# Performance work log

Measured on AMD Instinct MI355X. Metric: run time of the kernel, lower is better.

Reference implementation:

```python
import jax, jax.numpy as jnp
import numpy as np

K = 20
EPS = 1e-5
NEG_SLOPE = 0.2


def _graph_feature(x, k):
    # x: [B, N, C] -> edge features [B, N, k, 2C]
    xx = jnp.sum(x * x, axis=-1)                       # [B, N]
    inner = jnp.einsum('bnc,bmc->bnm', x, x)           # [B, N, N]
    neg_dist = 2.0 * inner - xx[:, :, None] - xx[:, None, :]
    idx = jax.lax.top_k(neg_dist, k)[1]                # [B, N, k] nearest neighbors
    nbr = jax.vmap(lambda f, i: f[i])(x, idx)          # [B, N, k, C]
    center = jnp.broadcast_to(x[:, :, None, :], nbr.shape)
    return jnp.concatenate([nbr - center, center], axis=-1)


def _bn(y, gamma, beta, axes):
    mu = y.mean(axes, keepdims=True)
    var = y.var(axes, keepdims=True)
    return (y - mu) * jax.lax.rsqrt(var + EPS) * gamma + beta


def _lrelu(y):
    return jnp.where(y > 0, y, NEG_SLOPE * y)


def _edge_block(feat, w, gamma, beta):
    # feat: [B, N, k, Cin], w: [Cout, Cin] (1x1 conv)
    y = jnp.einsum('bnkc,oc->bnko', feat, w)
    y = _lrelu(_bn(y, gamma, beta, (0, 1, 2)))
    return y.max(axis=2)                               # max over k -> [B, N, Cout]


def setup_inputs() -> dict:
    key = jax.random.key(0)
    ks = jax.random.split(key, 8)
    B, N = 16, 2048
    num_features = 128
    x = jax.random.normal(ks[0], (B, N, 3), dtype=jnp.float32)
    s = 0.05
    w1 = jax.random.normal(ks[1], (64, 6), dtype=jnp.float32) * s
    w2 = jax.random.normal(ks[2], (64, 128), dtype=jnp.float32) * s
    w3 = jax.random.normal(ks[3], (128, 128), dtype=jnp.float32) * s
    w4 = jax.random.normal(ks[4], (256, 256), dtype=jnp.float32) * s
    w5 = jax.random.normal(ks[5], (512, 512), dtype=jnp.float32) * s
    we = jax.random.normal(ks[6], (num_features, 512), dtype=jnp.float32) * s
    def gb(c):
        return jnp.ones((c,), jnp.float32), jnp.zeros((c,), jnp.float32)
    g1, b1 = gb(64); g2, b2 = gb(64); g3, b3 = gb(128); g4, b4 = gb(256); g5, b5 = gb(512)
    return dict(x=x, w1=w1, g1=g1, b1=b1, w2=w2, g2=g2, b2=b2, w3=w3, g3=g3, b3=b3,
                w4=w4, g4=g4, b4=b4, w5=w5, g5=g5, b5=b5, we=we)


def reference(x, w1, g1, b1, w2, g2, b2, w3, g3, b3, w4, g4, b4, w5, g5, b5, we):
    # x: [B, N, 3]
    x1 = _edge_block(_graph_feature(x, K), w1, g1, b1)    # [B, N, 64]
    x2 = _edge_block(_graph_feature(x1, K), w2, g2, b2)   # [B, N, 64]
    x3 = _edge_block(_graph_feature(x2, K), w3, g3, b3)   # [B, N, 128]
    x4 = _edge_block(_graph_feature(x3, K), w4, g4, b4)   # [B, N, 256]
    cat = jnp.concatenate([x1, x2, x3, x4], axis=-1)      # [B, N, 512]
    y = jnp.einsum('bnc,oc->bno', cat, w5)                # conv5 (1x1 conv1d)
    y = _lrelu(_bn(y, g5, b5, (0, 1)))
    y = y.max(axis=1)                                     # global max pool -> [B, 512]
    return y @ we.T                                       # embedding -> [B, num_features]
```

## Files before the change

### kernel.cpp

```cpp
#include <hip/hip_runtime.h>
#include <hip/hip_bf16.h>
#include <cstdint>

#define B_ 16
#define N_ 2048
#define KNN_K 20
#define EPS_ 1e-5f
#define SLOPE_ 0.2f

typedef __attribute__((ext_vector_type(4))) float f32x4;
typedef __attribute__((ext_vector_type(8))) short bf16x8;

static __device__ __forceinline__ float lrelu(float v){ return v > 0.f ? v : SLOPE_*v; }

static __device__ __forceinline__ unsigned encf(float f){
  unsigned b = __float_as_uint(f);
  return (b & 0x80000000u) ? ~b : (b | 0x80000000u);
}
static __device__ __forceinline__ float decf(unsigned u){
  unsigned b = (u & 0x80000000u) ? (u ^ 0x80000000u) : ~u;
  return __uint_as_float(b);
}
static __device__ __forceinline__ short bfbits(float v){
  __hip_bfloat16 h = __float2bfloat16(v);
  return *reinterpret_cast<short*>(&h);
}
static __device__ __forceinline__ float bf2f(short s){
  __hip_bfloat16 h = *reinterpret_cast<__hip_bfloat16*>(&s);
  return __bfloat162float(h);
}

template<int C, int CP>
__global__ __launch_bounds__(256) void convert_kernel(const float* __restrict__ f, int lda,
                                                      short* __restrict__ fbf, size_t plane,
                                                      float* __restrict__ xx){
  int wid  = (blockIdx.x * 256 + threadIdx.x) >> 6;
  int lane = threadIdx.x & 63;
  if (wid >= B_*N_) return;
  const float* p = f + (size_t)wid*lda;
  float s = 0.f;
  for (int c = lane; c < CP; c += 64){
    float v = (c < C) ? p[c] : 0.f;
    short h = bfbits(v);
    float r1 = v - bf2f(h);
    short m = bfbits(r1);
    short l = bfbits(r1 - bf2f(m));
    size_t o = (size_t)wid*CP + c;
    fbf[o] = h;
    fbf[plane + o] = m;
    fbf[2*plane + o] = l;
    s += v*v;
  }
  #pragma unroll
  for (int off=32; off; off>>=1) s += __shfl_down(s, off);
  if (lane==0) xx[wid] = s;
}

template<int CP>
__global__ __launch_bounds__(256) void knn_mfma(const short* __restrict__ fbf, size_t plane,
                                                const float* __restrict__ xx,
                                                int* __restrict__ idxout){
  constexpr int SP = (CP == 32) ? 72 : CP + 8;
  constexpr int CH = CP/8;
  constexpr int KC = CP/32;
  __shared__ short fmb[3*64*SP];
  __shared__ float xn_s[64], xm_s[64];
  __shared__ float dtile[64*65];

  int b   = blockIdx.x >> 5;
  int n0  = (blockIdx.x & 31) << 6;
  int tid = threadIdx.x;
  int w    = tid >> 6;
  int lane = tid & 63;
  int fr = lane & 15, hi = lane >> 4;
  int r_loc = lane >> 2, csub = lane & 3;
  int gb = lane & 60;
  int myrow = w*16 + r_loc;
  size_t browoff = (size_t)b * N_;

  bf16x8 aH[KC], aM[KC], aL[KC];
  {
    size_t arow = (browoff + n0 + w*16 + fr) * (size_t)CP;
    #pragma unroll
    for (int kc=0; kc<KC; ++kc){
      aH[kc] = *(const bf16x8*)&fbf[arow + kc*32 + hi*8];
      aM[kc] = *(const bf16x8*)&fbf[plane + arow + kc*32 + hi*8];
      aL[kc] = *(const bf16x8*)&fbf[2*plane + arow + kc*32 + hi*8];
    }
  }
  if (tid < 64) xn_s[tid] = xx[browoff + n0 + tid];

  float sv[5]; int si[5];
  #pragma unroll
  for (int j=0;j<5;++j){ sv[j] = -1e30f; si[j] = 0x7FFFFFFF; }

  for (int mt = 0; mt < N_/64; ++mt){
    __syncthreads();
    int m0 = mt << 6;
    for (int i = tid; i < 3*64*CH; i += 256){
      int p = i / (64*CH);
      int rem = i - p*64*CH;
      int r = rem / CH, cq = rem - r*CH;
      *(bf16x8*)&fmb[p*64*SP + r*SP + cq*8] =
          *(const bf16x8*)&fbf[(size_t)p*plane + (browoff + m0 + r)*(size_t)CP + cq*8];
    }
    if (tid < 64) xm_s[tid] = xx[browoff + m0 + tid];
    __syncthreads();

    f32x4 acc[4];
    #pragma unroll
    for (int ct=0; ct<4; ++ct) acc[ct] = (f32x4){0.f,0.f,0.f,0.f};
    const short* BH = fmb;
    const short* BM = fmb + 64*SP;
    const short* BL = fmb + 2*64*SP;
    #pragma unroll
    for (int kc = 0; kc < KC; ++kc){
      #pragma unroll
      for (int ct=0; ct<4; ++ct){
        int boff = (ct*16 + fr)*SP + kc*32 + hi*8;
        bf16x8 bh = *(const bf16x8*)&BH[boff];
        bf16x8 bm = *(const bf16x8*)&BM[boff];
        bf16x8 bl = *(const bf16x8*)&BL[boff];
        acc[ct] = __builtin_amdgcn_mfma_f32_16x16x32_bf16(aH[kc], bh, acc[ct], 0,0,0);
        acc[ct] = __builtin_amdgcn_mfma_f32_16x16x32_bf16(aM[kc], bh, acc[ct], 0,0,0);
        acc[ct] = __builtin_amdgcn_mfma_f32_16x16x32_bf16(aH[kc], bm, acc[ct], 0,0,0);
        acc[ct] = __builtin_amdgcn_mfma_f32_16x16x32_bf16(aM[kc], bm, acc[ct], 0,0,0);
        acc[ct] = __builtin_amdgcn_mfma_f32_16x16x32_bf16(aL[kc], bh, acc[ct], 0,0,0);
        acc[ct] = __builtin_amdgcn_mfma_f32_16x16x32_bf16(aH[kc], bl, acc[ct], 0,0,0);
      }
    }
    #pragma unroll
    for (int reg=0; reg<4; ++reg){
      int nl = w*16 + hi*4 + reg;
      float xn = xn_s[nl];
      #pragma unroll
      for (int ct=0; ct<4; ++ct)
        dtile[nl*65 + ct*16 + fr] = 2.f*acc[ct][reg] - xn - xm_s[ct*16 + fr];
    }

    int base = myrow*65 + csub*16;
    float thr = __shfl(sv[4], lane | 3);
    unsigned qm = 0u;
    #pragma unroll
    for (int jj=0; jj<16; ++jj){
      float v = dtile[base + jj];
      qm |= (v > thr) ? (1u << jj) : 0u;
    }
    unsigned long long bal = __ballot(qm != 0u);
    while (bal){
      unsigned nib = (unsigned)((bal >> gb) & 0xFull);
      int leader = nib ? (gb + (int)__builtin_ctz(nib)) : 64;
      int bbit = (int)__builtin_ctz(qm | 0x10000u);
      float mv = dtile[base + (bbit & 15)];
      int mid = m0 + (csub << 4) + bbit;
      float cv = __shfl(mv, leader);
      int   cid = __shfl(mid, leader);
      qm = (lane == leader) ? (qm & (qm - 1u)) : qm;
      int cnt = 0;
      #pragma unroll
      for (int j=0;j<5;++j) cnt += (sv[j] >= cv) ? 1 : 0;
      cnt += __shfl_xor(cnt, 1);
      cnt += __shfl_xor(cnt, 2);
      int pos = nib ? cnt : 20;
      float pv = __shfl_up(sv[4], 1);
      int   pi = __shfl_up(si[4], 1);
      #pragma unroll
      for (int j=0;j<5;++j){
        int g = csub*5 + j;
        float ns = (g < pos) ? sv[j] : ((g == pos) ? cv : pv);
        int   ni = (g < pos) ? si[j] : ((g == pos) ? cid : pi);
        pv = sv[j]; pi = si[j];
        sv[j] = ns; si[j] = ni;
      }
      bal = __ballot(qm != 0u);
    }
  }

  size_t orow = browoff + n0 + myrow;
  #pragma unroll
  for (int j=0;j<5;++j) idxout[orow*KNN_K + csub*5 + j] = si[j];
}

template<int CP>
__global__ __launch_bounds__(256) void gemm_pq(const short* __restrict__ fbf, size_t plane,
                                               const float* __restrict__ Wsrc, int wstride, int Cin,
                                               float* __restrict__ Out, int O){
  constexpr int BK = (CP < 64) ? CP : 64;
  constexpr int SP = BK + 8;
  __shared__ short Ah[128*SP];
  __shared__ short Am[128*SP];
  __shared__ short Wh[64*SP];
  __shared__ short Wm[64*SP];
  int obl = O >> 6;
  int bo = ((int)blockIdx.x % obl) << 6;
  int bm = ((int)blockIdx.x / obl) << 7;
  int tid = threadIdx.x;
  int w = tid >> 6, lane = tid & 63;
  int fr = lane & 15, hi = lane >> 4;
  f32x4 acc[2][4];
  #pragma unroll
  for (int g=0; g<2; ++g)
    #pragma unroll
    for (int ct=0; ct<4; ++ct) acc[g][ct] = (f32x4){0.f,0.f,0.f,0.f};

  for (int k0=0; k0<CP; k0+=BK){
    __syncthreads();
    for (int i=tid; i < 128*(BK/8); i += 256){
      int r = i/(BK/8), cq = i%(BK/8);
      size_t src = ((size_t)bm + r)*CP + k0 + cq*8;
      *(bf16x8*)&Ah[r*SP + cq*8] = *(const bf16x8*)&fbf[src];
      *(bf16x8*)&Am[r*SP + cq*8] = *(const bf16x8*)&fbf[plane + src];
    }
    for (int i=tid; i < 64*(BK/8); i += 256){
      int r = i/(BK/8), cq = i%(BK/8);
      bf16x8 vh, vm;
      #pragma unroll
      for (int e=0;e<8;++e){
        int c = k0 + cq*8 + e;
        float v = (c < Cin) ? Wsrc[(size_t)(bo + r)*wstride + c] : 0.f;
        short h = bfbits(v);
        vh[e] = h;
        vm[e] = bfbits(v - bf2f(h));
      }
      *(bf16x8*)&Wh[r*SP + cq*8] = vh;
      *(bf16x8*)&Wm[r*SP + cq*8] = vm;
    }
    __syncthreads();
    #pragma unroll
    for (int kc=0; kc<BK/32; ++kc){
      bf16x8 a0h = *(const bf16x8*)&Ah[(w*32 +      fr)*SP + kc*32 + hi*8];
      bf16x8 a0m = *(const bf16x8*)&Am[(w*32 +      fr)*SP + kc*32 + hi*8];
      bf16x8 a1h = *(const bf16x8*)&Ah[(w*32 + 16 + fr)*SP + kc*32 + hi*8];
      bf16x8 a1m = *(const bf16x8*)&Am[(w*32 + 16 + fr)*SP + kc*32 + hi*8];
      #pragma unroll
      for (int ct=0; ct<4; ++ct){
        bf16x8 bh = *(const bf16x8*)&Wh[(ct*16 + fr)*SP + kc*32 + hi*8];
        bf16x8 bm = *(const bf16x8*)&Wm[(ct*16 + fr)*SP + kc*32 + hi*8];
        acc[0][ct] = __builtin_amdgcn_mfma_f32_16x16x32_bf16(a0h, bh, acc[0][ct], 0,0,0);
        acc[0][ct] = __builtin_amdgcn_mfma_f32_16x16x32_bf16(a0m, bh, acc[0][ct], 0,0,0);
        acc[0][ct] = __builtin_amdgcn_mfma_f32_16x16x32_bf16(a0h, bm, acc[0][ct], 0,0,0);
        acc[1][ct] = __builtin_amdgcn_mfma_f32_16x16x32_bf16(a1h, bh, acc[1][ct], 0,0,0);
        acc[1][ct] = __builtin_amdgcn_mfma_f32_16x16x32_bf16(a1m, bh, acc[1][ct], 0,0,0);
        acc[1][ct] = __builtin_amdgcn_mfma_f32_16x16x32_bf16(a1h, bm, acc[1][ct], 0,0,0);
      }
    }
  }
  #pragma unroll
  for (int g=0; g<2; ++g)
    #pragma unroll
    for (int ct=0; ct<4; ++ct)
      #pragma unroll
      for (int reg=0; reg<4; ++reg){
        int row = bm + w*32 + g*16 + hi*4 + reg;
        Out[(size_t)row*O + bo + ct*16 + fr] = acc[g][ct][reg];
      }
}

__global__ __launch_bounds__(256) void gemm_bf16(const float* __restrict__ A,
                                                 const float* __restrict__ Wt,
                                                 float* __restrict__ C){
  __shared__ short As[128*72];
  __shared__ short Bs[64*72];
  int bm = (int)(blockIdx.x >> 3) << 7;
  int bo = (int)(blockIdx.x & 7) << 6;
  int tid = threadIdx.x;
  int w = tid >> 6, lane = tid & 63;
  int fr = lane & 15, hi = lane >> 4;
  f32x4 acc[2][4];
  #pragma unroll
  for (int g=0; g<2; ++g)
    #pragma unroll
    for (int ct=0; ct<4; ++ct) acc[g][ct] = (f32x4){0.f,0.f,0.f,0.f};

  for (int k0=0; k0<512; k0+=64){
    __syncthreads();
    #pragma unroll 2
    for (int i = tid; i < 1024; i += 256){
      int r = i >> 3, cq = i & 7;
      const float* src = &A[(size_t)(bm + r)*512 + k0 + cq*8];
      bf16x8 v;
      #pragma unroll
      for (int e=0;e<8;++e) v[e] = bfbits(src[e]);
      *(bf16x8*)&As[r*72 + cq*8] = v;
    }
    #pragma unroll 2
    for (int i = tid; i < 512; i += 256){
      int r = i >> 3, cq = i & 7;
      const float* src = &Wt[(size_t)(bo + r)*512 + k0 + cq*8];
      bf16x8 v;
      #pragma unroll
      for (int e=0;e<8;++e) v[e] = bfbits(src[e]);
      *(bf16x8*)&Bs[r*72 + cq*8] = v;
    }
    __syncthreads();
    #pragma unroll
    for (int kc=0; kc<2; ++kc){
      bf16x8 a0 = *(const bf16x8*)&As[(w*32 +      fr)*72 + kc*32 + hi*8];
      bf16x8 a1 = *(const bf16x8*)&As[(w*32 + 16 + fr)*72 + kc*32 + hi*8];
      #pragma unroll
      for (int ct=0; ct<4; ++ct){
        bf16x8 bb = *(const bf16x8*)&Bs[(ct*16 + fr)*72 + kc*32 + hi*8];
        acc[0][ct] = __builtin_amdgcn_mfma_f32_16x16x32_bf16(a0, bb, acc[0][ct], 0,0,0);
        acc[1][ct] = __builtin_amdgcn_mfma_f32_16x16x32_bf16(a1, bb, acc[1][ct], 0,0,0);
      }
    }
  }
  #pragma unroll
  for (int g=0; g<2; ++g)
    #pragma unroll
    for (int ct=0; ct<4; ++ct)
      #pragma unroll
      for (int reg=0; reg<4; ++reg){
        int row = bm + w*32 + g*16 + hi*4 + reg;
        C[(size_t)row*512 + bo + ct*16 + fr] = acc[g][ct][reg];
      }
}

__global__ void wq_kernel(const float* __restrict__ w, float* __restrict__ wq, int Cin, int O){
  int i = blockIdx.x*blockDim.x + threadIdx.x;
  if (i >= O*Cin) return;
  int o = i / Cin, c = i - o*Cin;
  wq[i] = w[(size_t)o*2*Cin + Cin + c] - w[(size_t)o*2*Cin + c];
}

__global__ void zero_f_kernel(float* p, int n){
  int i = blockIdx.x*blockDim.x + threadIdx.x;
  if (i < n) p[i] = 0.f;
}
__global__ void zero_u_kernel(unsigned* p, int n){
  int i = blockIdx.x*blockDim.x + threadIdx.x;
  if (i < n) p[i] = 0u;
}

__global__ __launch_bounds__(256) void edge_agg(const float* __restrict__ P, const float* __restrict__ Q,
      const int* __restrict__ idx, const float* __restrict__ gamma,
      float* __restrict__ S, float* __restrict__ sums, float* __restrict__ sumsq, int O){
  const int ROWS = 64;
  int rpi = 256 / O;
  int iters = ROWS / rpi;
  int row0 = blockIdx.x * ROWS;
  int tid = threadIdx.x;
  int o  = tid % O;
  int rl = tid / O;
  int b  = row0 / N_;
  __shared__ int sidx[4][KNN_K];
  __shared__ float s1[256], s2[256];
  float g = gamma[o];
  float csum=0.f, csumsq=0.f;
  for (int it=0; it<iters; ++it){
    __syncthreads();
    if (tid < KNN_K*rpi) sidx[tid/KNN_K][tid%KNN_K] = idx[(size_t)(row0 + it*rpi)*KNN_K + tid];
    __syncthreads();
    int row = row0 + it*rpi + rl;
    float q = Q[(size_t)row*O + o];
    float mx=-1e30f, mn=1e30f, s=0.f, ss=0.f;
    #pragma unroll
    for (int k=0;k<KNN_K;++k){
      int m = sidx[rl][k];
      float p = P[((size_t)b*N_ + m)*O + o];
      mx = fmaxf(mx,p); mn = fminf(mn,p);
      float y = p + q; s += y; ss += y*y;
    }
    csum += s; csumsq += ss;
    S[(size_t)row*O + o] = (g >= 0.f ? mx : mn) + q;
  }
  s1[tid]=0.f; s2[tid]=0.f;
  __syncthreads();
  atomicAdd(&s1[o], csum); atomicAdd(&s2[o], csumsq);
  __syncthreads();
  if (tid < O){ atomicAdd(&sums[tid], s1[tid]); atomicAdd(&sumsq[tid], s2[tid]); }
}

__global__ void bn_finalize(const float* __restrict__ sums, const float* __restrict__ sumsq,
                            const float* __restrict__ gamma, const float* __restrict__ beta,
                            float invM, float* __restrict__ scale, float* __restrict__ shift, int O){
  int o = blockIdx.x*blockDim.x + threadIdx.x;
  if (o >= O) return;
  float mu = sums[o]*invM;
  float var = sumsq[o]*invM - mu*mu;
  float rs = rsqrtf(var + EPS_);
  float sc = gamma[o]*rs;
  scale[o] = sc; shift[o] = beta[o] - mu*sc;
}

__global__ void apply_write(const float* __restrict__ S, const float* __restrict__ scale,
                            const float* __restrict__ shift, float* __restrict__ cat, int off, int O){
  int i = blockIdx.x*blockDim.x + threadIdx.x;
  if (i >= B_*N_*O) return;
  int row = i / O, o = i - row*O;
  float v = S[i]*scale[o] + shift[o];
  cat[(size_t)row*512 + off + o] = lrelu(v);
}

__global__ __launch_bounds__(256) void conv5_stats(const float* __restrict__ Y, const float* __restrict__ g5,
      float* __restrict__ sums, float* __restrict__ sumsq, unsigned* __restrict__ maxenc){
  int bb = blockIdx.x / 16;
  int n0 = (blockIdx.x % 16) * 128;
  int tid = threadIdx.x;
  float s0=0.f, s1=0.f, q0=0.f, q1=0.f, m0=-1e30f, m1=-1e30f;
  float ga = g5[tid], gb = g5[tid+256];
  for (int n=0;n<128;++n){
    size_t base = ((size_t)bb*N_ + n0 + n)*512;
    float ya = Y[base + tid];
    float yb = Y[base + tid + 256];
    s0 += ya; q0 += ya*ya;
    s1 += yb; q1 += yb*yb;
    m0 = fmaxf(m0, ga>=0.f ? ya : -ya);
    m1 = fmaxf(m1, gb>=0.f ? yb : -yb);
  }
  atomicAdd(&sums[tid],      s0); atomicAdd(&sumsq[tid],      q0);
  atomicAdd(&sums[tid+256],  s1); atomicAdd(&sumsq[tid+256],  q1);
  atomicMax(&maxenc[bb*512 + tid],       encf(m0));
  atomicMax(&maxenc[bb*512 + tid + 256], encf(m1));
}

__global__ void pool_kernel(const unsigned* __restrict__ maxenc, const float* __restrict__ scale,
                            const float* __restrict__ shift, const float* __restrict__ g5,
                            float* __restrict__ pooled){
  int i = blockIdx.x*blockDim.x + threadIdx.x;
  if (i >= B_*512) return;
  int o = i & 511;
  float t = decf(maxenc[i]);
  float y = g5[o] >= 0.f ? t : -t;
  pooled[i] = lrelu(y*scale[o] + shift[o]);
}

__global__ void final_mm(const float* __restrict__ pooled, const float* __restrict__ we,
                         float* __restrict__ out){
  int i = blockIdx.x*blockDim.x + threadIdx.x;
  if (i >= B_*128) return;
  int b = i >> 7, j = i & 127;
  const float4* pp = (const float4*)(pooled + (size_t)b*512);
  const float4* wp = (const float4*)(we + (size_t)j*512);
  float s = 0.f;
  for (int c=0;c<128;++c){
    float4 a = pp[c], w = wp[c];
    s += a.x*w.x + a.y*w.y + a.z*w.z + a.w*w.w;
  }
  out[i] = s;
}

struct Ws {
  float* cat; float* P; float* Q; float* S; int* idx; float* xx;
  float* sums; float* sumsq; float* scale; float* shift;
  float* wq; unsigned* maxenc; float* pooled; short* fbf;
};

template<int C, int CP>
static void run_layer(const Ws& W, const float* f, int lda, int O,
                      const float* w, const float* g, const float* bt,
                      int off_out, hipStream_t stream){
  const int M = B_*N_;
  size_t plane = (size_t)M*CP;
  convert_kernel<C, CP><<<M/4, 256, 0, stream>>>(f, lda, W.fbf, plane, W.xx);
  knn_mfma<CP><<<B_*(N_/64), 256, 0, stream>>>(W.fbf, plane, W.xx, W.idx);
  int nwq = O*C;
  wq_kernel<<<(nwq+255)/256, 256, 0, stream>>>(w, W.wq, C, O);
  int grid = (M/128)*(O/64);
  gemm_pq<CP><<<grid, 256, 0, stream>>>(W.fbf, plane, w,    2*C, C, W.P, O);
  gemm_pq<CP><<<grid, 256, 0, stream>>>(W.fbf, plane, W.wq, C,   C, W.Q, O);
  zero_f_kernel<<<4, 256, 0, stream>>>(W.sums, 1024);
  edge_agg<<<M/64, 256, 0, stream>>>(W.P, W.Q, W.idx, g, W.S, W.sums, W.sumsq, O);
  bn_finalize<<<(O+255)/256, 256, 0, stream>>>(W.sums, W.sumsq, g, bt,
                                               1.f/((float)M*KNN_K), W.scale, W.shift, O);
  apply_write<<<(M*O+255)/256, 256, 0, stream>>>(W.S, W.scale, W.shift, W.cat, off_out, O);
}

extern "C" void kernel_launch(void* const* d_in, const int* in_sizes, int n_in,
                              void* d_out, int out_size, void* d_ws, size_t ws_size,
                              hipStream_t stream) {
  const float* x  = (const float*)d_in[0];
  const float* w1 = (const float*)d_in[1];
  const float* g1 = (const float*)d_in[2];
  const float* b1 = (const float*)d_in[3];
  const float* w2 = (const float*)d_in[4];
  const float* g2 = (const float*)d_in[5];
  const float* b2 = (const float*)d_in[6];
  const float* w3 = (const float*)d_in[7];
  const float* g3 = (const float*)d_in[8];
  const float* b3 = (const float*)d_in[9];
  const float* w4 = (const float*)d_in[10];
  const float* g4 = (const float*)d_in[11];
  const float* b4 = (const float*)d_in[12];
  const float* w5 = (const float*)d_in[13];
  const float* g5 = (const float*)d_in[14];
  const float* b5 = (const float*)d_in[15];
  const float* we = (const float*)d_in[16];

  char* ws = (char*)d_ws;
  Ws W;
  size_t off = 0;
  W.cat   = (float*)(ws + off); off += (size_t)16*2048*512*4;
  W.P     = (float*)(ws + off); off += (size_t)16*2048*256*4;
  W.Q     = (float*)(ws + off); off += (size_t)16*2048*256*4;
  W.S     = (float*)(ws + off); off += (size_t)16*2048*256*4;
  W.idx   = (int*)  (ws + off); off += (size_t)16*2048*20*4;
  W.xx    = (float*)(ws + off); off += (size_t)16*2048*4;
  W.sums  = (float*)(ws + off); off += 512*4;
  W.sumsq = (float*)(ws + off); off += 512*4;
  W.scale = (float*)(ws + off); off += 512*4;
  W.shift = (float*)(ws + off); off += 512*4;
  W.wq    = (float*)(ws + off); off += (size_t)256*128*4;
  W.maxenc= (unsigned*)(ws + off); off += (size_t)16*512*4;
  W.pooled= (float*)(ws + off); off += (size_t)16*512*4;
  W.fbf   = (short*)W.S;

  const int M = B_*N_;

  run_layer<3,   32>(W, x,           3,   64,  w1, g1, b1, 0,   stream);
  run_layer<64,  64>(W, W.cat,       512, 64,  w2, g2, b2, 64,  stream);
  run_layer<64,  64>(W, W.cat + 64,  512, 128, w3, g3, b3, 128, stream);
  run_layer<128,128>(W, W.cat + 128, 512, 256, w4, g4, b4, 256, stream);

  float* y5 = W.P;
  gemm_bf16<<<(M/128)*8, 256, 0, stream>>>(W.cat, w5, y5);
  zero_f_kernel<<<4, 256, 0, stream>>>(W.sums, 1024);
  zero_u_kernel<<<32, 256, 0, stream>>>(W.maxenc, 16*512);
  conv5_stats<<<B_*16, 256, 0, stream>>>(y5, g5, W.sums, W.sumsq, W.maxenc);
  bn_finalize<<<2, 256, 0, stream>>>(W.sums, W.sumsq, g5, b5, 1.f/(float)M, W.scale, W.shift, 512);
  pool_kernel<<<(16*512+255)/256, 256, 0, stream>>>(W.maxenc, W.scale, W.shift, g5, W.pooled);
  final_mm<<<(16*128+255)/256, 256, 0, stream>>>(W.pooled, we, (float*)d_out);
}
```

Baseline: 1.271 ms.

## Split KNN candidate range across two blocks, prefetch tiles, and merge partial top-k

The KNN kernel now splits the candidate points of each query tile into two halves handled by separate blocks, which doubles the grid. Each block writes a partial top-20 list with values, and a new merge kernel combines the two sorted lists into the final indices. The tile loads are software-prefetched into registers while the MFMA work runs, the distance tile shares LDS with the feature buffer when it fits, and launch bounds request higher occupancy. The costs are an extra kernel launch, extra global traffic for the partial results, and more register pressure from the prefetch buffers.

```diff
diff --git a/kernel.cpp b/kernel.cpp
--- a/kernel.cpp
+++ b/kernel.cpp
@@ -57,18 +57,26 @@
 }
 
 template<int CP>
-__global__ __launch_bounds__(256) void knn_mfma(const short* __restrict__ fbf, size_t plane,
+__global__ __launch_bounds__(256, (CP==128)?3:4) void knn_mfma(const short* __restrict__ fbf, size_t plane,
                                                 const float* __restrict__ xx,
-                                                int* __restrict__ idxout){
-  constexpr int SP = (CP == 32) ? 72 : CP + 8;
+                                                float* __restrict__ pval, int* __restrict__ pidx){
+  constexpr int SP = CP + 8;
   constexpr int CH = CP/8;
   constexpr int KC = CP/32;
-  __shared__ short fmb[3*64*SP];
+  constexpr int PF = 3*CP/32;
+  constexpr int FMBS = 3*64*SP;
+  constexpr bool ALIAS = (FMBS*2 >= 64*65*4);
+  constexpr unsigned LDSB = ALIAS ? (unsigned)(FMBS*2) : (unsigned)(FMBS*2 + 64*65*4);
+  __shared__ __align__(16) char ldsbuf[LDSB];
+  short* fmb = (short*)ldsbuf;
+  float* dtile = ALIAS ? (float*)ldsbuf : (float*)(ldsbuf + FMBS*2);
   __shared__ float xn_s[64], xm_s[64];
-  __shared__ float dtile[64*65];
-
-  int b   = blockIdx.x >> 5;
-  int n0  = (blockIdx.x & 31) << 6;
+
+  int b   = blockIdx.x >> 6;
+  int rem = blockIdx.x & 63;
+  int n0  = (rem >> 1) << 6;
+  int mh  = rem & 1;
+  int mbase = mh << 10;
   int tid = threadIdx.x;
   int w    = tid >> 6;
   int lane = tid & 63;
@@ -94,18 +102,35 @@
   #pragma unroll
   for (int j=0;j<5;++j){ sv[j] = -1e30f; si[j] = 0x7FFFFFFF; }
 
-  for (int mt = 0; mt < N_/64; ++mt){
-    __syncthreads();
-    int m0 = mt << 6;
-    for (int i = tid; i < 3*64*CH; i += 256){
-      int p = i / (64*CH);
-      int rem = i - p*64*CH;
-      int r = rem / CH, cq = rem - r*CH;
-      *(bf16x8*)&fmb[p*64*SP + r*SP + cq*8] =
-          *(const bf16x8*)&fbf[(size_t)p*plane + (browoff + m0 + r)*(size_t)CP + cq*8];
-    }
-    if (tid < 64) xm_s[tid] = xx[browoff + m0 + tid];
-    __syncthreads();
+  bf16x8 pf[PF];
+  float xmreg = 0.f;
+  auto PFLOAD = [&](int mt){
+    int m0 = mbase + (mt<<6);
+    #pragma unroll
+    for (int j=0;j<PF;++j){
+      int i = tid + j*256;
+      int p = i/(64*CH); int rm = i - p*64*CH; int r = rm/CH, cq = rm - r*CH;
+      pf[j] = *(const bf16x8*)&fbf[(size_t)p*plane + (browoff + m0 + r)*(size_t)CP + cq*8];
+    }
+    if (tid < 64) xmreg = xx[browoff + m0 + tid];
+  };
+  auto WRITEPF = [&](){
+    #pragma unroll
+    for (int j=0;j<PF;++j){
+      int i = tid + j*256;
+      int p = i/(64*CH); int rm = i - p*64*CH; int r = rm/CH, cq = rm - r*CH;
+      *(bf16x8*)&fmb[p*64*SP + r*SP + cq*8] = pf[j];
+    }
+    if (tid < 64) xm_s[tid] = xmreg;
+  };
+
+  PFLOAD(0);
+  WRITEPF();
+  __syncthreads();
+
+  for (int mt = 0; mt < 16; ++mt){
+    int m0 = mbase + (mt << 6);
+    if (mt + 1 < 16) PFLOAD(mt + 1);
 
     f32x4 acc[4];
     #pragma unroll
@@ -129,6 +154,8 @@
         acc[ct] = __builtin_amdgcn_mfma_f32_16x16x32_bf16(aH[kc], bl, acc[ct], 0,0,0);
       }
     }
+    __syncthreads();
+
     #pragma unroll
     for (int reg=0; reg<4; ++reg){
       int nl = w*16 + hi*4 + reg;
@@ -174,11 +201,43 @@
       }
       bal = __ballot(qm != 0u);
     }
+
+    if (mt + 1 < 16){
+      if constexpr (ALIAS){
+        __syncthreads();
+        WRITEPF();
+        __syncthreads();
+      } else {
+        WRITEPF();
+        __syncthreads();
+      }
+    }
   }
 
   size_t orow = browoff + n0 + myrow;
-  #pragma unroll
-  for (int j=0;j<5;++j) idxout[orow*KNN_K + csub*5 + j] = si[j];
+  float* pvo = pval + (orow*2 + mh)*KNN_K + csub*5;
+  int*   pio = pidx + (orow*2 + mh)*KNN_K + csub*5;
+  #pragma unroll
+  for (int j=0;j<5;++j){ pvo[j] = sv[j]; pio[j] = si[j]; }
+}
+
+__global__ __launch_bounds__(256) void knn_merge(const float* __restrict__ pval,
+                                                 const int* __restrict__ pidx,
+                                                 int* __restrict__ idxout){
+  int r = blockIdx.x*256 + threadIdx.x;
+  if (r >= B_*N_) return;
+  const float* va = pval + (size_t)r*2*KNN_K;
+  const float* vb = va + KNN_K;
+  const int*   ia = pidx + (size_t)r*2*KNN_K;
+  const int*   ib = ia + KNN_K;
+  int i=0, j=0;
+  #pragma unroll
+  for (int t=0;t<KNN_K;++t){
+    float a = va[i], bq = vb[j];
+    bool ta = (a >= bq);
+    idxout[(size_t)r*KNN_K + t] = ta ? ia[i] : ib[j];
+    i += ta ? 1 : 0; j += ta ? 0 : 1;
+  }
 }
 
 template<int CP>
@@ -444,6 +503,7 @@
   float* cat; float* P; float* Q; float* S; int* idx; float* xx;
   float* sums; float* sumsq; float* scale; float* shift;
   float* wq; unsigned* maxenc; float* pooled; short* fbf;
+  float* pval; int* pidx;
 };
 
 template<int C, int CP>
@@ -453,7 +513,8 @@
   const int M = B_*N_;
   size_t plane = (size_t)M*CP;
   convert_kernel<C, CP><<<M/4, 256, 0, stream>>>(f, lda, W.fbf, plane, W.xx);
-  knn_mfma<CP><<<B_*(N_/64), 256, 0, stream>>>(W.fbf, plane, W.xx, W.idx);
+  knn_mfma<CP><<<B_*(N_/64)*2, 256, 0, stream>>>(W.fbf, plane, W.xx, W.pval, W.pidx);
+  knn_merge<<<(M+255)/256, 256, 0, stream>>>(W.pval, W.pidx, W.idx);
   int nwq = O*C;
   wq_kernel<<<(nwq+255)/256, 256, 0, stream>>>(w, W.wq, C, O);
   int grid = (M/128)*(O/64);
@@ -504,6 +565,8 @@
   W.maxenc= (unsigned*)(ws + off); off += (size_t)16*512*4;
   W.pooled= (float*)(ws + off); off += (size_t)16*512*4;
   W.fbf   = (short*)W.S;
+  W.pval  = W.Q;
+  W.pidx  = (int*)(W.Q + (size_t)2*16*2048*KNN_K);
 
   const int M = B_*N_;
 
```

After: 1.280 ms. No clear change (+0.7%).
